# Performance work log

Hardware: AMD Instinct MI355X
Metric: run time of the kernel (lower is better)

Reference implementation:

```python
import jax, jax.numpy as jnp
import numpy as np

H, W, WS = 48, 48, 8          # spatial grid and window radius
D, NUM_HEADS = 256, 8          # embed dim, heads
N = H * W
K = (2 * WS + 1) ** 2          # max neighbors = 289
EPS = 1e-5


def _precompute_neighbors(h, w, ws):
    """Faithful port of SCAM._precompute_neighbors (pads ragged rows with n[0])."""
    neighbors_list = []
    for idx in range(h * w):
        row, col = idx // w, idx % w
        nb = []
        for i in range(-ws, ws + 1):
            for j in range(-ws, ws + 1):
                r, c = row + i, col + j
                if 0 <= r < h and 0 <= c < w:
                    nb.append(r * w + c)
        neighbors_list.append(nb)
    max_n = max(len(n) for n in neighbors_list)
    padded = np.array([n + [n[0]] * (max_n - len(n)) for n in neighbors_list], dtype=np.int32)
    return padded


def setup_inputs() -> dict:
    key = jax.random.key(0)
    k1, k2, k3, k4 = jax.random.split(key, 4)
    B = 1
    scale = 0.02
    return {
        "x1": jax.random.normal(k1, (B, N, D), dtype=jnp.float32),
        "x2": jax.random.normal(k2, (B, N, D), dtype=jnp.float32),
        "ln_gamma": jnp.ones((D,), jnp.float32),
        "ln_beta": jnp.zeros((D,), jnp.float32),
        "in_proj_w": jax.random.normal(k3, (3 * D, D), dtype=jnp.float32) * scale,
        "in_proj_b": jnp.zeros((3 * D,), jnp.float32),
        "out_w": jax.random.normal(k4, (D, D), dtype=jnp.float32) * scale,
        "out_b": jnp.zeros((D,), jnp.float32),
        "neighbors_idx": jnp.asarray(_precompute_neighbors(H, W, WS)),  # [N, K] int32
    }


def _layernorm(x, gamma, beta):
    mu = jnp.mean(x, axis=-1, keepdims=True)
    var = jnp.var(x, axis=-1, keepdims=True)
    return (x - mu) * jax.lax.rsqrt(var + EPS) * gamma + beta


def reference(x1, x2, ln_gamma, ln_beta, in_proj_w, in_proj_b, out_w, out_b, neighbors_idx):
    B, n, d = x1.shape
    hd = d // NUM_HEADS

    # --- neighborhood gather-attention on x2 ---
    neighbor_feats = x2[:, neighbors_idx, :]                         # [B, N, K, D]
    scores = jnp.einsum('bnd,bnkd->bnk', x2, neighbor_feats) / (d ** 0.5)
    attn_w = jax.nn.softmax(scores, axis=-1)                          # softmax over neighbors
    x2_fused = jnp.einsum('bnk,bnkd->bnd', attn_w, neighbor_feats)    # [B, N, D]
    x2_fused = _layernorm(x2_fused, ln_gamma, ln_beta)

    # --- standard MHA: query=x2_fused, key=value=x1 ---
    wq, wk, wv = in_proj_w[:d], in_proj_w[d:2 * d], in_proj_w[2 * d:]
    bq, bk, bv = in_proj_b[:d], in_proj_b[d:2 * d], in_proj_b[2 * d:]
    q = (x2_fused @ wq.T + bq).reshape(B, n, NUM_HEADS, hd).transpose(0, 2, 1, 3)
    k = (x1 @ wk.T + bk).reshape(B, n, NUM_HEADS, hd).transpose(0, 2, 1, 3)
    v = (x1 @ wv.T + bv).reshape(B, n, NUM_HEADS, hd).transpose(0, 2, 1, 3)
    logits = jnp.einsum('bhqd,bhkd->bhqk', q, k) / (hd ** 0.5)        # [B, H, N, N]
    p = jax.nn.softmax(logits, axis=-1)
    o = jnp.einsum('bhqk,bhkd->bhqd', p, v)                           # [B, H, N, hd]
    o = o.transpose(0, 2, 1, 3).reshape(B, n, d)
    return o @ out_w.T + out_b
```

## Files before the change

kernel.cpp:

```cpp
#include <hip/hip_runtime.h>
#include <math.h>

#define N 2304
#define D 256
#define NH 8
#define HD 32
#define KS 8
#define SEG (N / KS)
#define NCH (SEG / 32)
#define NGR 2320

typedef __attribute__((ext_vector_type(8))) short short8;
typedef __attribute__((ext_vector_type(4))) short bf16x4;
typedef __attribute__((ext_vector_type(4))) float floatx4;

static __device__ __forceinline__ unsigned short f2bf(float x) {
  union { float f; unsigned u; } v; v.f = x;
  unsigned r = (v.u + 0x7fffu + ((v.u >> 16) & 1u)) >> 16;
  return (unsigned short)r;
}
static __device__ __forceinline__ float bf2f(unsigned short h) {
  union { unsigned u; float f; } v; v.u = (unsigned)h << 16;
  return v.f;
}
static __device__ __forceinline__ unsigned pack2bf(float lo, float hi) {
  return (unsigned)f2bf(lo) | ((unsigned)f2bf(hi) << 16);
}

struct Params {
  const float *x1, *x2, *lng, *lnb, *ipw, *ipb, *ow, *ob;
  float *out;
  float *pacc, *psum;
  unsigned short *Qb, *Kb, *Vtb;
  unsigned short *x2b_full, *x2t_full;
  unsigned short *wh, *wl, *owh, *owl;
};

__global__ __launch_bounds__(256) void prep_kernel(Params P)
{
  __shared__ unsigned short T[16][17];
  const int t = threadIdx.x, bid = blockIdx.x, NB = gridDim.x;
  for (int i = bid * 256 + t; i < 262144; i += NB * 256) {
    const float* src; unsigned short *dh, *dl; int off;
    if (i < 196608) { src = P.ipw; dh = P.wh;  dl = P.wl;  off = i; }
    else            { src = P.ow;  dh = P.owh; dl = P.owl; off = i - 196608; }
    const float v = src[off];
    const unsigned short h = f2bf(v);
    dh[off] = h;
    dl[off] = f2bf(v - bf2f(h));
  }
  const int tx = t & 15, ty = t >> 4;
  for (int u = bid; u < 145 * 16; u += NB) {
    const int k0 = (u % 145) * 16, f0 = (u / 145) * 16;
    const int key = k0 + ty - 8;
    unsigned short v = 0;
    if (key >= 0 && key < N) v = f2bf(P.x2[(size_t)key * D + f0 + tx]);
    P.x2b_full[(size_t)(k0 + ty) * D + f0 + tx] = v;
    T[ty][tx] = v;
    __syncthreads();
    P.x2t_full[(size_t)(f0 + ty) * NGR + k0 + tx] = T[tx][ty];
    __syncthreads();
  }
}

__global__ __launch_bounds__(256) void mid_kernel(Params P)
{
  __shared__ __align__(16) unsigned short Pb[16 * 552];
  __shared__ __align__(16) unsigned short xfh[16 * 264];
  __shared__ __align__(16) unsigned short xfl[16 * 264];
  __shared__ float dn[64], lr1[64], lr2[64];

  const int bid  = blockIdx.x;
  const int t    = threadIdx.x;
  const int wv   = t >> 6;
  const int lane = t & 63;
  const int g    = lane >> 4;
  const int c    = lane & 15;
  const unsigned short* x2b = P.x2b_full + 8 * D;
  const unsigned short* x2t = P.x2t_full + 8;

  if (bid < 144) {
    const int r  = bid / 3;
    const int c0 = (bid % 3) * 16;
    const int qbase  = r * 48 + c0;
    const int row_lo = max(0, 8 - r);
    const int row_hi = min(16, 55 - r);
    const int nrows  = min(r + 8, 47) - max(r - 8, 0) + 1;

    short8 qf[8];
    {
      const unsigned short* qptr = x2b + (size_t)(qbase + c) * D + g * 8;
      #pragma unroll
      for (int si = 0; si < 8; ++si) qf[si] = *(const short8*)(qptr + si * 32);
    }

    float pssum[4] = {0.f, 0.f, 0.f, 0.f};
    for (int wr = row_lo + wv; wr <= row_hi; wr += 4) {
      const int kr = r - 8 + wr;
      const int keybase = kr * 48 + c0 - 8;
      #pragma unroll
      for (int ch = 0; ch < 2; ++ch) {
        const unsigned short* kptr = x2b + (size_t)(keybase + ch * 16 + c) * D + g * 8;
        floatx4 sa = {0.f, 0.f, 0.f, 0.f};
        #pragma unroll
        for (int si = 0; si < 8; ++si) {
          const short8 kf = *(const short8*)(kptr + si * 32);
          sa = __builtin_amdgcn_mfma_f32_16x16x32_bf16(qf[si], kf, sa, 0, 0, 0);
        }
        const int wc = ch * 16 + c;
        const int kc_img = c0 - 8 + wc;
        #pragma unroll
        for (int reg = 0; reg < 4; ++reg) {
          const int qi = g * 4 + reg;
          float sv = sa[reg] * 0.0625f;
          const int cimg  = c0 + qi;
          const int ncols = min(cimg + 8, 47) - max(cimg - 8, 0) + 1;
          const int mult  = 289 - nrows * ncols + 1;
          const int wc0q  = (cimg >= 8) ? qi : (8 - c0);
          if (mult > 1 && wr == row_lo && wc == wc0q) sv += __logf((float)mult);
          const bool valid = (kc_img >= 0) & (kc_img < 48) &
                             (wc >= qi) & (wc <= qi + 16);
          const float pv = valid ? __expf(sv) : 0.f;
          pssum[reg] += pv;
          Pb[qi * 552 + wr * 32 + wc] = valid ? f2bf(pv) : (unsigned short)0;
        }
      }
    }
    #pragma unroll
    for (int off = 1; off <= 8; off <<= 1) {
      #pragma unroll
      for (int reg = 0; reg < 4; ++reg) pssum[reg] += __shfl_xor(pssum[reg], off);
    }
    if (c == 0) {
      #pragma unroll
      for (int reg = 0; reg < 4; ++reg) dn[wv * 16 + g * 4 + reg] = pssum[reg];
    }
    __syncthreads();

    floatx4 acc[4];
    #pragma unroll
    for (int ng = 0; ng < 4; ++ng) acc[ng] = (floatx4){0.f, 0.f, 0.f, 0.f};
    const int fb = wv * 64;
    for (int wr = row_lo; wr <= row_hi; ++wr) {
      const int keybase = (r - 8 + wr) * 48 + c0 - 8;
      const short8 pA = *(const short8*)&Pb[c * 552 + wr * 32 + g * 8];
      #pragma unroll
      for (int ng = 0; ng < 4; ++ng) {
        const short8 vf = *(const short8*)(x2t + (size_t)(fb + ng * 16 + c) * NGR + keybase + g * 8);
        acc[ng] = __builtin_amdgcn_mfma_f32_16x16x32_bf16(pA, vf, acc[ng], 0, 0, 0);
      }
    }

    float vout[4][4], ps1[4] = {0,0,0,0}, ps2[4] = {0,0,0,0};
    #pragma unroll
    for (int reg = 0; reg < 4; ++reg) {
      const int m = g * 4 + reg;
      const float di = 1.f / (dn[m] + dn[16 + m] + dn[32 + m] + dn[48 + m]);
      #pragma unroll
      for (int ng = 0; ng < 4; ++ng) {
        const float v = acc[ng][reg] * di;
        vout[ng][reg] = v;
        ps1[reg] += v;
        ps2[reg] += v * v;
      }
    }
    #pragma unroll
    for (int off = 1; off <= 8; off <<= 1) {
      #pragma unroll
      for (int reg = 0; reg < 4; ++reg) {
        ps1[reg] += __shfl_xor(ps1[reg], off);
        ps2[reg] += __shfl_xor(ps2[reg], off);
      }
    }
    if (c == 0) {
      #pragma unroll
      for (int reg = 0; reg < 4; ++reg) {
        lr1[wv * 16 + g * 4 + reg] = ps1[reg];
        lr2[wv * 16 + g * 4 + reg] = ps2[reg];
      }
    }
    __syncthreads();
    #pragma unroll
    for (int reg = 0; reg < 4; ++reg) {
      const int m = g * 4 + reg;
      const float s1 = lr1[m] + lr1[16 + m] + lr1[32 + m] + lr1[48 + m];
      const float s2 = lr2[m] + lr2[16 + m] + lr2[32 + m] + lr2[48 + m];
      const float mu  = s1 * (1.f / 256.f);
      const float var = s2 * (1.f / 256.f) - mu * mu;
      const float rs  = rsqrtf(var + 1e-5f);
      #pragma unroll
      for (int ng = 0; ng < 4; ++ng) {
        const int f = fb + ng * 16 + c;
        const float val = (vout[ng][reg] - mu) * rs * P.lng[f] + P.lnb[f];
        const unsigned short h = f2bf(val);
        xfh[m * 264 + f] = h;
        xfl[m * 264 + f] = f2bf(val - bf2f(h));
      }
    }
    __syncthreads();

    const int nw = wv * 64;
    floatx4 qacc[4];
    #pragma unroll
    for (int nt = 0; nt < 4; ++nt) qacc[nt] = (floatx4){0.f, 0.f, 0.f, 0.f};
    for (int kc = 0; kc < 256; kc += 32) {
      const short8 ah = *(const short8*)&xfh[c * 264 + kc + g * 8];
      const short8 al = *(const short8*)&xfl[c * 264 + kc + g * 8];
      #pragma unroll
      for (int nt = 0; nt < 4; ++nt) {
        const short8 bh = *(const short8*)(P.wh + (size_t)(nw + nt * 16 + c) * 256 + kc + g * 8);
        const short8 bl = *(const short8*)(P.wl + (size_t)(nw + nt * 16 + c) * 256 + kc + g * 8);
        qacc[nt] = __builtin_amdgcn_mfma_f32_16x16x32_bf16(ah, bh, qacc[nt], 0, 0, 0);
        qacc[nt] = __builtin_amdgcn_mfma_f32_16x16x32_bf16(al, bh, qacc[nt], 0, 0, 0);
        qacc[nt] = __builtin_amdgcn_mfma_f32_16x16x32_bf16(ah, bl, qacc[nt], 0, 0, 0);
      }
    }
    const float qscale = 0.17677669529663687f;
    #pragma unroll
    for (int nt = 0; nt < 4; ++nt) {
      const int j = nw + nt * 16 + c;
      const float bj = P.ipb[j];
      #pragma unroll
      for (int reg = 0; reg < 4; ++reg) {
        const int m = qbase + 4 * g + reg;
        P.Qb[(size_t)m * 256 + j] = f2bf((qacc[nt][reg] + bj) * qscale);
      }
    }
  } else if (bid < 288) {
    const int idx = bid - 144;
    const int m0  = (idx >> 2) * 64;
    const int nw  = 256 + (idx & 3) * 128 + wv * 32;
    floatx4 acc[4][2];
    #pragma unroll
    for (int mt = 0; mt < 4; ++mt)
      #pragma unroll
      for (int nt = 0; nt < 2; ++nt) acc[mt][nt] = (floatx4){0.f, 0.f, 0.f, 0.f};

    for (int kc = 0; kc < 256; kc += 32) {
      short8 ah[4], al[4];
      #pragma unroll
      for (int mt = 0; mt < 4; ++mt) {
        const float* xp = P.x1 + (size_t)(m0 + mt * 16 + c) * 256 + kc + g * 8;
        const float4 va = *(const float4*)xp;
        const float4 vb = *(const float4*)(xp + 4);
        const float vv[8] = {va.x, va.y, va.z, va.w, vb.x, vb.y, vb.z, vb.w};
        #pragma unroll
        for (int e = 0; e < 8; ++e) {
          const unsigned short h = f2bf(vv[e]);
          ah[mt][e] = (short)h;
          al[mt][e] = (short)f2bf(vv[e] - bf2f(h));
        }
      }
      short8 bh[2], bl[2];
      #pragma unroll
      for (int nt = 0; nt < 2; ++nt) {
        bh[nt] = *(const short8*)(P.wh + (size_t)(nw + nt * 16 + c) * 256 + kc + g * 8);
        bl[nt] = *(const short8*)(P.wl + (size_t)(nw + nt * 16 + c) * 256 + kc + g * 8);
      }
      #pragma unroll
      for (int mt = 0; mt < 4; ++mt)
        #pragma unroll
        for (int nt = 0; nt < 2; ++nt) {
          acc[mt][nt] = __builtin_amdgcn_mfma_f32_16x16x32_bf16(ah[mt], bh[nt], acc[mt][nt], 0, 0, 0);
          acc[mt][nt] = __builtin_amdgcn_mfma_f32_16x16x32_bf16(al[mt], bh[nt], acc[mt][nt], 0, 0, 0);
          acc[mt][nt] = __builtin_amdgcn_mfma_f32_16x16x32_bf16(ah[mt], bl[nt], acc[mt][nt], 0, 0, 0);
        }
    }
    #pragma unroll
    for (int mt = 0; mt < 4; ++mt)
      #pragma unroll
      for (int nt = 0; nt < 2; ++nt) {
        const int j = nw + nt * 16 + c;
        const float bj = P.ipb[j];
        #pragma unroll
        for (int rr = 0; rr < 4; ++rr) {
          const int m = m0 + mt * 16 + 4 * g + rr;
          const float v = acc[mt][nt][rr] + bj;
          if (j < 512) P.Kb[(size_t)m * 256 + (j - 256)] = f2bf(v);
          else         P.Vtb[(size_t)(j - 512) * N + m] = f2bf(v);
        }
      }
  }
}

__global__ __launch_bounds__(128) void attn_kernel(Params P)
{
  __shared__ __align__(16) unsigned short Ksh[2][32 * 40];
  __shared__ __align__(16) unsigned short Vsh[2][32 * 40];

  const int t    = threadIdx.x;
  const int wv   = t >> 6;
  const int lane = t & 63;
  const int g    = lane >> 4;
  const int c    = lane & 15;
  const int seg  = blockIdx.x;
  const int qb   = blockIdx.y;
  const int head = blockIdx.z;
  const int q0w  = qb * 128 + wv * 64;
  const int key0 = seg * SEG;

  short8 qf[4];
  #pragma unroll
  for (int qt = 0; qt < 4; ++qt)
    qf[qt] = *(const short8*)(P.Qb + (size_t)(q0w + qt * 16 + c) * D + head * HD + g * 8);

  const unsigned short* ksrc = P.Kb  + (size_t)(key0 + t / 4) * D + head * HD + (t % 4) * 8;
  const unsigned short* vsrc = P.Vtb + (size_t)(head * HD + t / 4) * N + key0 + (t % 4) * 8;
  const int sdst = (t / 4) * 40 + (t % 4) * 8;

  {
    const float4 gk = *(const float4*)ksrc;
    const float4 gv = *(const float4*)vsrc;
    *(float4*)&Ksh[0][sdst] = gk;
    *(float4*)&Vsh[0][sdst] = gv;
  }
  __syncthreads();

  floatx4 accL[4], accH[4];
  float ssum[4];
  #pragma unroll
  for (int qt = 0; qt < 4; ++qt) {
    accL[qt] = (floatx4){0.f, 0.f, 0.f, 0.f};
    accH[qt] = (floatx4){0.f, 0.f, 0.f, 0.f};
    ssum[qt] = 0.f;
  }

  for (int ch = 0; ch < NCH; ++ch) {
    float4 gk, gv;
    const bool more = (ch + 1 < NCH);
    if (more) {
      gk = *(const float4*)(ksrc + (size_t)(ch + 1) * 32 * D);
      gv = *(const float4*)(vsrc + (ch + 1) * 32);
    }
    const unsigned short* kb = Ksh[ch & 1];
    const unsigned short* vb = Vsh[ch & 1];

    #pragma unroll
    for (int kk = 0; kk < 2; ++kk) {
      const short8 kf  = *(const short8*)&kb[(kk * 16 + c) * 40 + g * 8];
      const bf16x4 vf0 = *(const bf16x4*)&vb[c * 40 + kk * 16 + g * 4];
      const bf16x4 vf1 = *(const bf16x4*)&vb[(16 + c) * 40 + kk * 16 + g * 4];
      #pragma unroll
      for (int qt = 0; qt < 4; ++qt) {
        const floatx4 z = {0.f, 0.f, 0.f, 0.f};
        floatx4 sA = __builtin_amdgcn_mfma_f32_16x16x32_bf16(kf, qf[qt], z, 0, 0, 0);
        const float p0 = __expf(sA[0]);
        const float p1 = __expf(sA[1]);
        const float p2 = __expf(sA[2]);
        const float p3 = __expf(sA[3]);
        ssum[qt] += (p0 + p1) + (p2 + p3);
        union { unsigned u[2]; bf16x4 s; } pB;
        pB.u[0] = pack2bf(p0, p1);
        pB.u[1] = pack2bf(p2, p3);
        accL[qt] = __builtin_amdgcn_mfma_f32_16x16x16bf16_1k(vf0, pB.s, accL[qt], 0, 0, 0);
        accH[qt] = __builtin_amdgcn_mfma_f32_16x16x16bf16_1k(vf1, pB.s, accH[qt], 0, 0, 0);
      }
    }
    if (more) {
      *(float4*)&Ksh[(ch + 1) & 1][sdst] = gk;
      *(float4*)&Vsh[(ch + 1) & 1][sdst] = gv;
    }
    __syncthreads();
  }

  #pragma unroll
  for (int qt = 0; qt < 4; ++qt) {
    float s = ssum[qt];
    s += __shfl_xor(s, 16);
    s += __shfl_xor(s, 32);
    const size_t row = (size_t)(seg * NH + head) * N + q0w + qt * 16 + c;
    *(float4*)(P.pacc + row * HD + g * 4) =
        make_float4(accL[qt][0], accL[qt][1], accL[qt][2], accL[qt][3]);
    *(float4*)(P.pacc + row * HD + 16 + g * 4) =
        make_float4(accH[qt][0], accH[qt][1], accH[qt][2], accH[qt][3]);
    if (g == 0) P.psum[row] = s;
  }
}

__global__ __launch_bounds__(256) void tail_kernel(Params P)
{
  __shared__ __align__(16) unsigned short oht[32 * 264];
  __shared__ __align__(16) unsigned short olt[32 * 264];
  const int bid  = blockIdx.x;
  const int t    = threadIdx.x;
  const int wv   = t >> 6;
  const int lane = t & 63;
  const int g    = lane >> 4;
  const int c    = lane & 15;
  const int m0 = bid * 32;
  {
    const int row = t >> 3;
    const int hh  = t & 7;
    const int mrow = m0 + row;
    float den = 0.f;
    #pragma unroll
    for (int sgi = 0; sgi < KS; ++sgi)
      den += P.psum[(size_t)(sgi * NH + hh) * N + mrow];
    const float dinv = 1.f / den;
    #pragma unroll
    for (int c4 = 0; c4 < 8; ++c4) {
      float ax = 0.f, ay = 0.f, az = 0.f, aw = 0.f;
      #pragma unroll
      for (int sgi = 0; sgi < KS; ++sgi) {
        const float4 pv = *(const float4*)&P.pacc[((size_t)(sgi * NH + hh) * N + mrow) * HD + c4 * 4];
        ax += pv.x; ay += pv.y; az += pv.z; aw += pv.w;
      }
      const int f0 = hh * 32 + c4 * 4;
      const float vv[4] = {ax * dinv, ay * dinv, az * dinv, aw * dinv};
      #pragma unroll
      for (int e = 0; e < 4; ++e) {
        const unsigned short h = f2bf(vv[e]);
        oht[row * 264 + f0 + e] = h;
        olt[row * 264 + f0 + e] = f2bf(vv[e] - bf2f(h));
      }
    }
  }
  __syncthreads();

  const int nw = wv * 64;
  floatx4 acc[2][4];
  #pragma unroll
  for (int mt = 0; mt < 2; ++mt)
    #pragma unroll
    for (int nt = 0; nt < 4; ++nt) acc[mt][nt] = (floatx4){0.f, 0.f, 0.f, 0.f};
  #pragma unroll
  for (int pass = 0; pass < 3; ++pass) {
    const unsigned short* Ap = (pass == 1) ? olt : oht;
    const unsigned short* Wp = (pass == 2) ? P.owl : P.owh;
    #pragma unroll
    for (int kc = 0; kc < 256; kc += 32) {
      short8 af[2], bf[4];
      #pragma unroll
      for (int mt = 0; mt < 2; ++mt)
        af[mt] = *(const short8*)&Ap[(mt * 16 + c) * 264 + kc + g * 8];
      #pragma unroll
      for (int nt = 0; nt < 4; ++nt)
        bf[nt] = *(const short8*)(Wp + (size_t)(nw + nt * 16 + c) * 256 + kc + g * 8);
      #pragma unroll
      for (int mt = 0; mt < 2; ++mt)
        #pragma unroll
        for (int nt = 0; nt < 4; ++nt)
          acc[mt][nt] = __builtin_amdgcn_mfma_f32_16x16x32_bf16(af[mt], bf[nt], acc[mt][nt], 0, 0, 0);
    }
  }
  #pragma unroll
  for (int mt = 0; mt < 2; ++mt)
    #pragma unroll
    for (int nt = 0; nt < 4; ++nt) {
      const int j = nw + nt * 16 + c;
      const float bj = P.ob[j];
      #pragma unroll
      for (int rr = 0; rr < 4; ++rr) {
        const int m = m0 + mt * 16 + 4 * g + rr;
        P.out[(size_t)m * 256 + j] = acc[mt][nt][rr] + bj;
      }
    }
}

extern "C" void kernel_launch(void* const* d_in, const int* in_sizes, int n_in,
                              void* d_out, int out_size, void* d_ws, size_t ws_size,
                              hipStream_t stream)
{
  (void)in_sizes; (void)n_in; (void)out_size; (void)ws_size;
  Params P;
  P.x1  = (const float*)d_in[0];
  P.x2  = (const float*)d_in[1];
  P.lng = (const float*)d_in[2];
  P.lnb = (const float*)d_in[3];
  P.ipw = (const float*)d_in[4];
  P.ipb = (const float*)d_in[5];
  P.ow  = (const float*)d_in[6];
  P.ob  = (const float*)d_in[7];
  P.out = (float*)d_out;

  char* p = (char*)d_ws;
  P.pacc = (float*)p;          p += (size_t)KS * NH * N * HD * 4;
  P.psum = (float*)p;          p += (size_t)KS * NH * N * 4;
  P.Qb   = (unsigned short*)p; p += (size_t)N * D * 2;
  P.Kb   = (unsigned short*)p; p += (size_t)N * D * 2;
  P.Vtb  = (unsigned short*)p; p += (size_t)D * N * 2;
  P.x2b_full = (unsigned short*)p; p += (size_t)NGR * D * 2;
  P.x2t_full = (unsigned short*)p; p += (size_t)D * NGR * 2;
  P.wh   = (unsigned short*)p; p += (size_t)768 * 256 * 2;
  P.wl   = (unsigned short*)p; p += (size_t)768 * 256 * 2;
  P.owh  = (unsigned short*)p; p += (size_t)256 * 256 * 2;
  P.owl  = (unsigned short*)p; p += (size_t)256 * 256 * 2;

  prep_kernel<<<288, 256, 0, stream>>>(P);
  mid_kernel<<<288, 256, 0, stream>>>(P);
  attn_kernel<<<dim3(KS, N / 128, NH), 128, 0, stream>>>(P);
  tail_kernel<<<72, 256, 0, stream>>>(P);
}
```

Measured before the change: 159.7 us.

## Pre-split x1 to bf16 hi/lo in prep, widen mid kernel to 8 waves with prefetch

The x1 hi/lo bf16 split moves out of the K/V projection blocks into prep_kernel, which now writes x1h/x1l buffers. mid_kernel goes from 256 to 512 threads and from 288 to 216 blocks. Each neighborhood-attention block now has 8 waves that split the window rows and feature columns, and each K/V block covers 256 output columns. Software prefetch (double buffering) of the next K-chunk operands is added to the PV, Q-projection and K/V-projection loops. This is meant to cut the per-block conversion ALU work and hide load latency, at the cost of extra global traffic for the x1 split buffers and more register pressure.

```diff
diff --git a/kernel.cpp b/kernel.cpp
--- a/kernel.cpp
+++ b/kernel.cpp
@@ -33,17 +33,18 @@
   float *pacc, *psum;
   unsigned short *Qb, *Kb, *Vtb;
   unsigned short *x2b_full, *x2t_full;
-  unsigned short *wh, *wl, *owh, *owl;
+  unsigned short *x1h, *x1l, *wh, *wl, *owh, *owl;
 };
 
 __global__ __launch_bounds__(256) void prep_kernel(Params P)
 {
   __shared__ unsigned short T[16][17];
   const int t = threadIdx.x, bid = blockIdx.x, NB = gridDim.x;
-  for (int i = bid * 256 + t; i < 262144; i += NB * 256) {
+  for (int i = bid * 256 + t; i < 851968; i += NB * 256) {
     const float* src; unsigned short *dh, *dl; int off;
-    if (i < 196608) { src = P.ipw; dh = P.wh;  dl = P.wl;  off = i; }
-    else            { src = P.ow;  dh = P.owh; dl = P.owl; off = i - 196608; }
+    if (i < 589824)      { src = P.x1;  dh = P.x1h; dl = P.x1l; off = i; }
+    else if (i < 786432) { src = P.ipw; dh = P.wh;  dl = P.wl;  off = i - 589824; }
+    else                 { src = P.ow;  dh = P.owh; dl = P.owl; off = i - 786432; }
     const float v = src[off];
     const unsigned short h = f2bf(v);
     dh[off] = h;
@@ -63,16 +64,16 @@
   }
 }
 
-__global__ __launch_bounds__(256) void mid_kernel(Params P)
+__global__ __launch_bounds__(512) void mid_kernel(Params P)
 {
   __shared__ __align__(16) unsigned short Pb[16 * 552];
   __shared__ __align__(16) unsigned short xfh[16 * 264];
   __shared__ __align__(16) unsigned short xfl[16 * 264];
-  __shared__ float dn[64], lr1[64], lr2[64];
+  __shared__ float dn[128], lr1[128], lr2[128];
 
   const int bid  = blockIdx.x;
   const int t    = threadIdx.x;
-  const int wv   = t >> 6;
+  const int w    = t >> 6;
   const int lane = t & 63;
   const int g    = lane >> 4;
   const int c    = lane & 15;
@@ -95,24 +96,32 @@
     }
 
     float pssum[4] = {0.f, 0.f, 0.f, 0.f};
-    for (int wr = row_lo + wv; wr <= row_hi; wr += 4) {
-      const int kr = r - 8 + wr;
-      const int keybase = kr * 48 + c0 - 8;
+    for (int wr = row_lo + w; wr <= row_hi; wr += 8) {
+      const int keybase = (r - 8 + wr) * 48 + c0 - 8;
+      const unsigned short* kp0 = x2b + (size_t)(keybase + c) * D + g * 8;
+      const unsigned short* kp1 = x2b + (size_t)(keybase + 16 + c) * D + g * 8;
+      short8 kA[8], kB[8];
+      #pragma unroll
+      for (int si = 0; si < 8; ++si) {
+        kA[si] = *(const short8*)(kp0 + si * 32);
+        kB[si] = *(const short8*)(kp1 + si * 32);
+      }
+      floatx4 sa = {0.f, 0.f, 0.f, 0.f};
+      floatx4 sb = {0.f, 0.f, 0.f, 0.f};
+      #pragma unroll
+      for (int si = 0; si < 8; ++si) {
+        sa = __builtin_amdgcn_mfma_f32_16x16x32_bf16(qf[si], kA[si], sa, 0, 0, 0);
+        sb = __builtin_amdgcn_mfma_f32_16x16x32_bf16(qf[si], kB[si], sb, 0, 0, 0);
+      }
       #pragma unroll
       for (int ch = 0; ch < 2; ++ch) {
-        const unsigned short* kptr = x2b + (size_t)(keybase + ch * 16 + c) * D + g * 8;
-        floatx4 sa = {0.f, 0.f, 0.f, 0.f};
-        #pragma unroll
-        for (int si = 0; si < 8; ++si) {
-          const short8 kf = *(const short8*)(kptr + si * 32);
-          sa = __builtin_amdgcn_mfma_f32_16x16x32_bf16(qf[si], kf, sa, 0, 0, 0);
-        }
+        const floatx4 sv4 = ch ? sb : sa;
         const int wc = ch * 16 + c;
         const int kc_img = c0 - 8 + wc;
         #pragma unroll
         for (int reg = 0; reg < 4; ++reg) {
           const int qi = g * 4 + reg;
-          float sv = sa[reg] * 0.0625f;
+          float sv = sv4[reg] * 0.0625f;
           const int cimg  = c0 + qi;
           const int ncols = min(cimg + 8, 47) - max(cimg - 8, 0) + 1;
           const int mult  = 289 - nrows * ncols + 1;
@@ -133,36 +142,46 @@
     }
     if (c == 0) {
       #pragma unroll
-      for (int reg = 0; reg < 4; ++reg) dn[wv * 16 + g * 4 + reg] = pssum[reg];
+      for (int reg = 0; reg < 4; ++reg) dn[w * 16 + g * 4 + reg] = pssum[reg];
     }
     __syncthreads();
 
-    floatx4 acc[4];
-    #pragma unroll
-    for (int ng = 0; ng < 4; ++ng) acc[ng] = (floatx4){0.f, 0.f, 0.f, 0.f};
-    const int fb = wv * 64;
-    for (int wr = row_lo; wr <= row_hi; ++wr) {
-      const int keybase = (r - 8 + wr) * 48 + c0 - 8;
-      const short8 pA = *(const short8*)&Pb[c * 552 + wr * 32 + g * 8];
-      #pragma unroll
-      for (int ng = 0; ng < 4; ++ng) {
-        const short8 vf = *(const short8*)(x2t + (size_t)(fb + ng * 16 + c) * NGR + keybase + g * 8);
-        acc[ng] = __builtin_amdgcn_mfma_f32_16x16x32_bf16(pA, vf, acc[ng], 0, 0, 0);
-      }
-    }
-
-    float vout[4][4], ps1[4] = {0,0,0,0}, ps2[4] = {0,0,0,0};
+    floatx4 acc0 = {0.f, 0.f, 0.f, 0.f};
+    floatx4 acc1 = {0.f, 0.f, 0.f, 0.f};
+    const int fb = w * 32;
+    const unsigned short* vrow0 = x2t + (size_t)(fb + c) * NGR;
+    const unsigned short* vrow1 = x2t + (size_t)(fb + 16 + c) * NGR;
+    {
+      int wr = row_lo;
+      int kb = (r - 8 + wr) * 48 + c0 - 8 + g * 8;
+      short8 pA = *(const short8*)&Pb[c * 552 + wr * 32 + g * 8];
+      short8 v0 = *(const short8*)(vrow0 + kb);
+      short8 v1 = *(const short8*)(vrow1 + kb);
+      for (; wr <= row_hi; ++wr) {
+        const int wn  = (wr < row_hi) ? wr + 1 : row_lo;
+        const int kbn = (r - 8 + wn) * 48 + c0 - 8 + g * 8;
+        short8 pAn = *(const short8*)&Pb[c * 552 + wn * 32 + g * 8];
+        short8 v0n = *(const short8*)(vrow0 + kbn);
+        short8 v1n = *(const short8*)(vrow1 + kbn);
+        acc0 = __builtin_amdgcn_mfma_f32_16x16x32_bf16(pA, v0, acc0, 0, 0, 0);
+        acc1 = __builtin_amdgcn_mfma_f32_16x16x32_bf16(pA, v1, acc1, 0, 0, 0);
+        pA = pAn; v0 = v0n; v1 = v1n;
+      }
+    }
+
+    float vout[2][4], ps1[4] = {0,0,0,0}, ps2[4] = {0,0,0,0};
     #pragma unroll
     for (int reg = 0; reg < 4; ++reg) {
       const int m = g * 4 + reg;
-      const float di = 1.f / (dn[m] + dn[16 + m] + dn[32 + m] + dn[48 + m]);
-      #pragma unroll
-      for (int ng = 0; ng < 4; ++ng) {
-        const float v = acc[ng][reg] * di;
-        vout[ng][reg] = v;
-        ps1[reg] += v;
-        ps2[reg] += v * v;
-      }
+      float den = 0.f;
+      #pragma unroll
+      for (int ww = 0; ww < 8; ++ww) den += dn[ww * 16 + m];
+      const float di = 1.f / den;
+      const float v0 = acc0[reg] * di;
+      const float v1 = acc1[reg] * di;
+      vout[0][reg] = v0; vout[1][reg] = v1;
+      ps1[reg] += v0 + v1;
+      ps2[reg] += v0 * v0 + v1 * v1;
     }
     #pragma unroll
     for (int off = 1; off <= 8; off <<= 1) {
@@ -175,21 +194,22 @@
     if (c == 0) {
       #pragma unroll
       for (int reg = 0; reg < 4; ++reg) {
-        lr1[wv * 16 + g * 4 + reg] = ps1[reg];
-        lr2[wv * 16 + g * 4 + reg] = ps2[reg];
+        lr1[w * 16 + g * 4 + reg] = ps1[reg];
+        lr2[w * 16 + g * 4 + reg] = ps2[reg];
       }
     }
     __syncthreads();
     #pragma unroll
     for (int reg = 0; reg < 4; ++reg) {
       const int m = g * 4 + reg;
-      const float s1 = lr1[m] + lr1[16 + m] + lr1[32 + m] + lr1[48 + m];
-      const float s2 = lr2[m] + lr2[16 + m] + lr2[32 + m] + lr2[48 + m];
+      float s1 = 0.f, s2 = 0.f;
+      #pragma unroll
+      for (int ww = 0; ww < 8; ++ww) { s1 += lr1[ww * 16 + m]; s2 += lr2[ww * 16 + m]; }
       const float mu  = s1 * (1.f / 256.f);
       const float var = s2 * (1.f / 256.f) - mu * mu;
       const float rs  = rsqrtf(var + 1e-5f);
       #pragma unroll
-      for (int ng = 0; ng < 4; ++ng) {
+      for (int ng = 0; ng < 2; ++ng) {
         const int f = fb + ng * 16 + c;
         const float val = (vout[ng][reg] - mu) * rs * P.lng[f] + P.lnb[f];
         const unsigned short h = f2bf(val);
@@ -199,63 +219,87 @@
     }
     __syncthreads();
 
-    const int nw = wv * 64;
-    floatx4 qacc[4];
-    #pragma unroll
-    for (int nt = 0; nt < 4; ++nt) qacc[nt] = (floatx4){0.f, 0.f, 0.f, 0.f};
+    const int nw = w * 32;
+    const unsigned short* bh0p = P.wh + (size_t)(nw + c) * 256 + g * 8;
+    const unsigned short* bh1p = P.wh + (size_t)(nw + 16 + c) * 256 + g * 8;
+    const unsigned short* bl0p = P.wl + (size_t)(nw + c) * 256 + g * 8;
+    const unsigned short* bl1p = P.wl + (size_t)(nw + 16 + c) * 256 + g * 8;
+    floatx4 q0 = {0.f, 0.f, 0.f, 0.f};
+    floatx4 q1 = {0.f, 0.f, 0.f, 0.f};
+    short8 bh0 = *(const short8*)bh0p;
+    short8 bh1 = *(const short8*)bh1p;
+    short8 bl0 = *(const short8*)bl0p;
+    short8 bl1 = *(const short8*)bl1p;
     for (int kc = 0; kc < 256; kc += 32) {
+      const int kn = (kc + 32 < 256) ? kc + 32 : 0;
+      short8 nbh0 = *(const short8*)(bh0p + kn);
+      short8 nbh1 = *(const short8*)(bh1p + kn);
+      short8 nbl0 = *(const short8*)(bl0p + kn);
+      short8 nbl1 = *(const short8*)(bl1p + kn);
       const short8 ah = *(const short8*)&xfh[c * 264 + kc + g * 8];
       const short8 al = *(const short8*)&xfl[c * 264 + kc + g * 8];
-      #pragma unroll
-      for (int nt = 0; nt < 4; ++nt) {
-        const short8 bh = *(const short8*)(P.wh + (size_t)(nw + nt * 16 + c) * 256 + kc + g * 8);
-        const short8 bl = *(const short8*)(P.wl + (size_t)(nw + nt * 16 + c) * 256 + kc + g * 8);
-        qacc[nt] = __builtin_amdgcn_mfma_f32_16x16x32_bf16(ah, bh, qacc[nt], 0, 0, 0);
-        qacc[nt] = __builtin_amdgcn_mfma_f32_16x16x32_bf16(al, bh, qacc[nt], 0, 0, 0);
-        qacc[nt] = __builtin_amdgcn_mfma_f32_16x16x32_bf16(ah, bl, qacc[nt], 0, 0, 0);
-      }
+      q0 = __builtin_amdgcn_mfma_f32_16x16x32_bf16(ah, bh0, q0, 0, 0, 0);
+      q0 = __builtin_amdgcn_mfma_f32_16x16x32_bf16(al, bh0, q0, 0, 0, 0);
+      q0 = __builtin_amdgcn_mfma_f32_16x16x32_bf16(ah, bl0, q0, 0, 0, 0);
+      q1 = __builtin_amdgcn_mfma_f32_16x16x32_bf16(ah, bh1, q1, 0, 0, 0);
+      q1 = __builtin_amdgcn_mfma_f32_16x16x32_bf16(al, bh1, q1, 0, 0, 0);
+      q1 = __builtin_amdgcn_mfma_f32_16x16x32_bf16(ah, bl1, q1, 0, 0, 0);
+      bh0 = nbh0; bh1 = nbh1; bl0 = nbl0; bl1 = nbl1;
     }
     const float qscale = 0.17677669529663687f;
     #pragma unroll
-    for (int nt = 0; nt < 4; ++nt) {
+    for (int nt = 0; nt < 2; ++nt) {
       const int j = nw + nt * 16 + c;
       const float bj = P.ipb[j];
+      const floatx4 qa = nt ? q1 : q0;
       #pragma unroll
       for (int reg = 0; reg < 4; ++reg) {
         const int m = qbase + 4 * g + reg;
-        P.Qb[(size_t)m * 256 + j] = f2bf((qacc[nt][reg] + bj) * qscale);
-      }
-    }
-  } else if (bid < 288) {
+        P.Qb[(size_t)m * 256 + j] = f2bf((qa[reg] + bj) * qscale);
+      }
+    }
+  } else if (bid < 216) {
     const int idx = bid - 144;
-    const int m0  = (idx >> 2) * 64;
-    const int nw  = 256 + (idx & 3) * 128 + wv * 32;
+    const int m0  = (idx >> 1) * 64;
+    const int nw  = 256 + (idx & 1) * 256 + w * 32;
     floatx4 acc[4][2];
     #pragma unroll
     for (int mt = 0; mt < 4; ++mt)
       #pragma unroll
       for (int nt = 0; nt < 2; ++nt) acc[mt][nt] = (floatx4){0.f, 0.f, 0.f, 0.f};
 
+    const unsigned short* ahp[4];
+    const unsigned short* alp[4];
+    #pragma unroll
+    for (int mt = 0; mt < 4; ++mt) {
+      ahp[mt] = P.x1h + (size_t)(m0 + mt * 16 + c) * 256 + g * 8;
+      alp[mt] = P.x1l + (size_t)(m0 + mt * 16 + c) * 256 + g * 8;
+    }
+    const unsigned short* bhp[2];
+    const unsigned short* blp[2];
+    #pragma unroll
+    for (int nt = 0; nt < 2; ++nt) {
+      bhp[nt] = P.wh + (size_t)(nw + nt * 16 + c) * 256 + g * 8;
+      blp[nt] = P.wl + (size_t)(nw + nt * 16 + c) * 256 + g * 8;
+    }
+    short8 ah[4], al[4], bh[2], bl[2];
+    #pragma unroll
+    for (int mt = 0; mt < 4; ++mt) { ah[mt] = *(const short8*)ahp[mt]; al[mt] = *(const short8*)alp[mt]; }
+    #pragma unroll
+    for (int nt = 0; nt < 2; ++nt) { bh[nt] = *(const short8*)bhp[nt]; bl[nt] = *(const short8*)blp[nt]; }
+
     for (int kc = 0; kc < 256; kc += 32) {
-      short8 ah[4], al[4];
+      const int kn = (kc + 32 < 256) ? kc + 32 : 0;
+      short8 nah[4], nal[4], nbh[2], nbl[2];
       #pragma unroll
       for (int mt = 0; mt < 4; ++mt) {
-        const float* xp = P.x1 + (size_t)(m0 + mt * 16 + c) * 256 + kc + g * 8;
-        const float4 va = *(const float4*)xp;
-        const float4 vb = *(const float4*)(xp + 4);
-        const float vv[8] = {va.x, va.y, va.z, va.w, vb.x, vb.y, vb.z, vb.w};
-        #pragma unroll
-        for (int e = 0; e < 8; ++e) {
-          const unsigned short h = f2bf(vv[e]);
-          ah[mt][e] = (short)h;
-          al[mt][e] = (short)f2bf(vv[e] - bf2f(h));
-        }
-      }
-      short8 bh[2], bl[2];
+        nah[mt] = *(const short8*)(ahp[mt] + kn);
+        nal[mt] = *(const short8*)(alp[mt] + kn);
+      }
       #pragma unroll
       for (int nt = 0; nt < 2; ++nt) {
-        bh[nt] = *(const short8*)(P.wh + (size_t)(nw + nt * 16 + c) * 256 + kc + g * 8);
-        bl[nt] = *(const short8*)(P.wl + (size_t)(nw + nt * 16 + c) * 256 + kc + g * 8);
+        nbh[nt] = *(const short8*)(bhp[nt] + kn);
+        nbl[nt] = *(const short8*)(blp[nt] + kn);
       }
       #pragma unroll
       for (int mt = 0; mt < 4; ++mt)
@@ -265,6 +309,10 @@
           acc[mt][nt] = __builtin_amdgcn_mfma_f32_16x16x32_bf16(al[mt], bh[nt], acc[mt][nt], 0, 0, 0);
           acc[mt][nt] = __builtin_amdgcn_mfma_f32_16x16x32_bf16(ah[mt], bl[nt], acc[mt][nt], 0, 0, 0);
         }
+      #pragma unroll
+      for (int mt = 0; mt < 4; ++mt) { ah[mt] = nah[mt]; al[mt] = nal[mt]; }
+      #pragma unroll
+      for (int nt = 0; nt < 2; ++nt) { bh[nt] = nbh[nt]; bl[nt] = nbl[nt]; }
     }
     #pragma unroll
     for (int mt = 0; mt < 4; ++mt)
@@ -481,13 +529,15 @@
   P.Vtb  = (unsigned short*)p; p += (size_t)D * N * 2;
   P.x2b_full = (unsigned short*)p; p += (size_t)NGR * D * 2;
   P.x2t_full = (unsigned short*)p; p += (size_t)D * NGR * 2;
+  P.x1h  = (unsigned short*)p; p += (size_t)N * D * 2;
+  P.x1l  = (unsigned short*)p; p += (size_t)N * D * 2;
   P.wh   = (unsigned short*)p; p += (size_t)768 * 256 * 2;
   P.wl   = (unsigned short*)p; p += (size_t)768 * 256 * 2;
   P.owh  = (unsigned short*)p; p += (size_t)256 * 256 * 2;
   P.owl  = (unsigned short*)p; p += (size_t)256 * 256 * 2;
 
   prep_kernel<<<288, 256, 0, stream>>>(P);
-  mid_kernel<<<288, 256, 0, stream>>>(P);
+  mid_kernel<<<216, 512, 0, stream>>>(P);
   attn_kernel<<<dim3(KS, N / 128, NH), 128, 0, stream>>>(P);
   tail_kernel<<<72, 256, 0, stream>>>(P);
 }
```

New measurement: 155.1 us. -2.9%, faster.
